# Kernel tuning notes

Hardware: AMD Instinct MI355X
Metric: run time of the kernel (lower is better)

Reference implementation:

```python
import jax, jax.numpy as jnp
import numpy as np

K_NN = 3  # pointnet2 relation default k=3


def setup_inputs() -> dict:
    key = jax.random.key(0)
    k1, k2, k3 = jax.random.split(key, 3)
    B, N, S, C = 4, 16384, 4096, 256
    q = jax.random.normal(k1, (B, N, 3), dtype=jnp.float32)
    k = jax.random.normal(k2, (B, S, 3), dtype=jnp.float32)
    v = jax.random.normal(k3, (B, S, C), dtype=jnp.float32)
    return {"q": q, "k": k, "v": v}


def reference(q, k, v):
    # squared pairwise distance: ||q||^2 - 2 q.k + ||k||^2  -> [B, N, S]
    d = (
        jnp.sum(q * q, axis=-1, keepdims=True)
        - 2.0 * jnp.einsum("bnd,bsd->bns", q, k)
        + jnp.sum(k * k, axis=-1)[:, None, :]
    )
    # 3 nearest neighbors (smallest distances)
    neg_d, idx = jax.lax.top_k(-d, K_NN)          # [B, N, 3]
    dists = -neg_d
    recip = 1.0 / (dists + 1e-8)
    weight = recip / jnp.sum(recip, axis=-1, keepdims=True)  # [B, N, 3]
    # score is zero except at idx; scatter+dense matmul == gather-weighted sum
    B = q.shape[0]
    vg = v[jnp.arange(B)[:, None, None], idx]     # [B, N, 3, C]
    extract = jnp.einsum("bnk,bnkc->bnc", weight, vg)  # [B, N, C]
    return jnp.transpose(extract, (0, 2, 1))      # [B, C, N] (embed is identity)
```

## Files before the change

### kernel.cpp

```cpp
#include <hip/hip_runtime.h>

#define BB 4
#define NN 16384
#define SS 4096
#define CC 256
#define TLD 132

typedef float f32x4 __attribute__((ext_vector_type(4)));

__device__ __forceinline__ bool lexlt(float da, int ia, float db, int ib) {
  return (da < db) || ((da == db) && (ia < ib));
}

#define DIST(kp) ({                                        \
  float _dot = (qx * (kp).x + qy * (kp).y) + qz * (kp).z;  \
  __builtin_fmaf(_dot, -2.0f, qq) + (kp).w;                \
})

#define INSERT(dd, ss) do {                                \
  bool _k2 = (dd) < d2, _k1 = (dd) < d1, _k0 = (dd) < d0;  \
  float _nd2 = __builtin_amdgcn_fmed3f((dd), d1, d2);      \
  float _nd1 = __builtin_amdgcn_fmed3f((dd), d0, d1);      \
  float _nd0 = fminf((dd), d0);                            \
  i2 = _k1 ? i1 : (_k2 ? (ss) : i2);                       \
  i1 = _k0 ? i0 : (_k1 ? (ss) : i1);                       \
  i0 = _k0 ? (ss) : i0;                                    \
  d2 = _nd2; d1 = _nd1; d0 = _nd0;                         \
} while (0)

__global__ __launch_bounds__(256, 8) void scan_kernel(
    const float* __restrict__ qg, const float* __restrict__ kg,
    float4* __restrict__ dpart, int4* __restrict__ ipart) {
#pragma clang fp contract(off)
  __shared__ __align__(16) float4 kpts[1024];
  float* md = (float*)kpts;
  int* mi = (int*)((char*)kpts + 1536);

  const int tid = threadIdx.x;
  const int blk = blockIdx.x;
  const int b = blk >> 9;
  const int seg = (blk >> 7) & 3;
  const int n0 = (blk & 127) << 7;
  const int wv = tid >> 6;
  const int lane = tid & 63;
  const int qg2 = wv & 1;
  const int half = wv >> 1;
  const int q = n0 + qg2 * 64 + lane;

  {
    const float* kb = kg + ((long)b * SS + (long)seg * 1024) * 3;
    const float4* src = (const float4*)kb + tid * 3;
    float4 f0 = src[0], f1 = src[1], f2 = src[2];
    float px[4] = {f0.x, f0.w, f1.z, f2.y};
    float py[4] = {f0.y, f1.x, f1.w, f2.z};
    float pz[4] = {f0.z, f1.y, f2.x, f2.w};
#pragma unroll
    for (int m = 0; m < 4; ++m) {
      float kk = (px[m] * px[m] + py[m] * py[m]) + pz[m] * pz[m];
      kpts[tid * 4 + m] = make_float4(px[m], py[m], pz[m], kk);
    }
  }

  const float* qp = qg + ((long)b * NN + q) * 3;
  float qx = qp[0], qy = qp[1], qz = qp[2];
  float qq = (qx * qx + qy * qy) + qz * qz;
  float d0 = 3.4e38f, d1 = 3.4e38f, d2 = 3.4e38f;
  int i0 = 0, i1 = 0, i2 = 0;
  __syncthreads();

  const int sb = seg * 1024;
  const int cbase = half << 9;

  for (int bdl = 0; bdl < 32; ++bdl) {
    const int base = cbase + (bdl << 4);
    const float tau = d2;
    float dv[16];
    unsigned msk = 0;
#pragma unroll
    for (int sj = 0; sj < 4; ++sj) {
      float4 ka = kpts[base + 4 * sj + 0];
      float4 kb_ = kpts[base + 4 * sj + 1];
      float4 kc = kpts[base + 4 * sj + 2];
      float4 kd = kpts[base + 4 * sj + 3];
      dv[4 * sj + 0] = DIST(ka);
      dv[4 * sj + 1] = DIST(kb_);
      dv[4 * sj + 2] = DIST(kc);
      dv[4 * sj + 3] = DIST(kd);
    }
#pragma unroll
    for (int j = 0; j < 16; ++j) msk |= (__any(dv[j] < tau) ? 1u : 0u) << j;
    if (msk) {
#pragma unroll
      for (int j = 0; j < 16; ++j) {
        if (msk & (1u << j)) INSERT(dv[j], sb + base + j);
      }
    }
  }

  __syncthreads();
  if (half == 1) {
    int basei = (qg2 * 64 + lane) * 3;
    md[basei + 0] = d0; md[basei + 1] = d1; md[basei + 2] = d2;
    mi[basei + 0] = i0; mi[basei + 1] = i1; mi[basei + 2] = i2;
  }
  __syncthreads();
  if (half == 0) {
    int basei = (qg2 * 64 + lane) * 3;
    float E0 = md[basei + 0], E1 = md[basei + 1], E2 = md[basei + 2];
    int F0 = mi[basei + 0], F1 = mi[basei + 1], F2 = mi[basei + 2];
    float A0 = d0, A1 = d1, A2 = d2;
    int B0 = i0, B1 = i1, B2 = i2;
    bool t = lexlt(E0, F0, A0, B0);
    float r0 = t ? E0 : A0; int s0 = t ? F0 : B0;
    float nA0 = t ? A0 : A1, nA1 = t ? A1 : A2;
    int nB0 = t ? B0 : B1, nB1 = t ? B1 : B2;
    float nE0 = t ? E1 : E0, nE1 = t ? E2 : E1;
    int nF0 = t ? F1 : F0, nF1 = t ? F2 : F1;
    bool u = lexlt(nE0, nF0, nA0, nB0);
    float r1 = u ? nE0 : nA0; int s1 = u ? nF0 : nB0;
    float mA0 = u ? nA0 : nA1; int mB0 = u ? nB0 : nB1;
    float mE0 = u ? nE1 : nE0; int mF0 = u ? nF1 : nF0;
    bool w = lexlt(mE0, mF0, mA0, mB0);
    float r2 = w ? mE0 : mA0; int s2 = w ? mF0 : mB0;
    long gid = (long)b * NN + q;
    dpart[gid * 4 + seg] = make_float4(r0, r1, r2, 0.0f);
    ipart[gid * 4 + seg] = make_int4(s0, s1, s2, 0);
  }
}

__global__ __launch_bounds__(256, 4) void gather_kernel(
    const float* __restrict__ vg, const float4* __restrict__ dpart,
    const int4* __restrict__ ipart, float* __restrict__ outg) {
#pragma clang fp contract(off)
  __shared__ __align__(16) float tile[64 * TLD];
  __shared__ float sw[64][3];
  __shared__ int si[64][3];

  const int tid = threadIdx.x;
  const int bid = blockIdx.x;
  const int xcd = bid & 7;
  const int b = xcd >> 1;
  const int chunk = xcd & 1;
  const int nblk = bid >> 3;
  const int n0 = nblk << 6;

  if (tid < 64) {
    long gid = (long)b * NN + n0 + tid;
    float D0 = 3.4e38f, D1 = 3.4e38f, D2 = 3.4e38f;
    int I0 = -1, I1 = -1, I2 = -1;
#pragma unroll
    for (int seg = 0; seg < 4; ++seg) {
      float4 dv = dpart[gid * 4 + seg];
      int4 iv = ipart[gid * 4 + seg];
      float ds_[3] = {dv.x, dv.y, dv.z};
      int is_[3] = {iv.x, iv.y, iv.z};
      for (int r = 0; r < 3; ++r) {
        float d = ds_[r];
        int s = is_[r];
        if (lexlt(d, s, D2, I2)) {
          if (lexlt(d, s, D1, I1)) {
            D2 = D1; I2 = I1;
            if (lexlt(d, s, D0, I0)) { D1 = D0; I1 = I0; D0 = d; I0 = s; }
            else { D1 = d; I1 = s; }
          } else { D2 = d; I2 = s; }
        }
      }
    }
    float r0 = 1.0f / (D0 + 1e-8f);
    float r1 = 1.0f / (D1 + 1e-8f);
    float r2 = 1.0f / (D2 + 1e-8f);
    float rs = (r0 + r1) + r2;
    sw[tid][0] = r0 / rs; sw[tid][1] = r1 / rs; sw[tid][2] = r2 / rs;
    si[tid][0] = I0; si[tid][1] = I1; si[tid][2] = I2;
  }
  __syncthreads();

  const int wv = tid >> 6;
  const int lane = tid & 63;
  const int qh = lane >> 5;
  const int slot = lane & 31;
  const float* vb = vg + (long)b * SS * CC + chunk * 128;

#pragma unroll 4
  for (int it = 0; it < 8; ++it) {
    int qs = wv * 16 + it * 2 + qh;
    float w0 = sw[qs][0], w1 = sw[qs][1], w2 = sw[qs][2];
    const float4* r0p = (const float4*)(vb + (long)si[qs][0] * CC);
    const float4* r1p = (const float4*)(vb + (long)si[qs][1] * CC);
    const float4* r2p = (const float4*)(vb + (long)si[qs][2] * CC);
    float4 a0 = r0p[slot], a1 = r1p[slot], a2 = r2p[slot];
    float4 acc;
    acc.x = (w0 * a0.x + w1 * a1.x) + w2 * a2.x;
    acc.y = (w0 * a0.y + w1 * a1.y) + w2 * a2.y;
    acc.z = (w0 * a0.z + w1 * a1.z) + w2 * a2.z;
    acc.w = (w0 * a0.w + w1 * a1.w) + w2 * a2.w;
    *(float4*)&tile[qs * TLD + slot * 4] = acc;
  }
  __syncthreads();

  {
    const int nf = tid & 15;
    const int cb0 = tid >> 4;
    const int q0 = nf << 2;
#pragma unroll 2
    for (int it = 0; it < 8; ++it) {
      int cl = cb0 + it * 16;
      int cch = (chunk << 7) + cl;
      f32x4 val;
      val.x = tile[(q0 + 0) * TLD + cl];
      val.y = tile[(q0 + 1) * TLD + cl];
      val.z = tile[(q0 + 2) * TLD + cl];
      val.w = tile[(q0 + 3) * TLD + cl];
      __builtin_nontemporal_store(
          val, (f32x4*)&outg[((long)(b * CC + cch)) * NN + n0 + q0]);
    }
  }
}

extern "C" void kernel_launch(void* const* d_in, const int* in_sizes, int n_in,
                              void* d_out, int out_size, void* d_ws, size_t ws_size,
                              hipStream_t stream) {
  const float* q = (const float*)d_in[0];
  const float* k = (const float*)d_in[1];
  const float* v = (const float*)d_in[2];
  float* out = (float*)d_out;
  float4* dpart = (float4*)d_ws;
  int4* ipart = (int4*)((char*)d_ws + (size_t)BB * NN * 4 * 16);
  hipLaunchKernelGGL(scan_kernel, dim3(2048), dim3(256), 0, stream, q, k, dpart, ipart);
  hipLaunchKernelGGL(gather_kernel, dim3(2048), dim3(256), 0, stream, v, dpart, ipart, out);
}
```

Measured before the change: 212.0 us.

## Process two queries per thread in scan kernel to reuse LDS key loads

Each thread in the kNN scan kernel now handles two query points instead of one, so every key point read from shared memory is used for two distance computations. The grid is halved to 1024 blocks, each covering 256 queries, and the shared merge buffers are resized. This cuts LDS load traffic and per-block key staging in half, at the cost of more registers (launch bounds relaxed to 4 blocks per CU), lower occupancy and fewer blocks to fill the GPU.

New measurement: 225.6 us. +6.4%, slower.

```diff
diff --git a/kernel.cpp b/kernel.cpp
--- a/kernel.cpp
+++ b/kernel.cpp
@@ -12,40 +12,41 @@
   return (da < db) || ((da == db) && (ia < ib));
 }
 
-#define DIST(kp) ({                                        \
-  float _dot = (qx * (kp).x + qy * (kp).y) + qz * (kp).z;  \
-  __builtin_fmaf(_dot, -2.0f, qq) + (kp).w;                \
+#define DIST3(QX, QY, QZ, QQ, kp) ({                            \
+  float _dot = ((QX) * (kp).x + (QY) * (kp).y) + (QZ) * (kp).z; \
+  __builtin_fmaf(_dot, -2.0f, (QQ)) + (kp).w;                   \
 })
 
-#define INSERT(dd, ss) do {                                \
-  bool _k2 = (dd) < d2, _k1 = (dd) < d1, _k0 = (dd) < d0;  \
-  float _nd2 = __builtin_amdgcn_fmed3f((dd), d1, d2);      \
-  float _nd1 = __builtin_amdgcn_fmed3f((dd), d0, d1);      \
-  float _nd0 = fminf((dd), d0);                            \
-  i2 = _k1 ? i1 : (_k2 ? (ss) : i2);                       \
-  i1 = _k0 ? i0 : (_k1 ? (ss) : i1);                       \
-  i0 = _k0 ? (ss) : i0;                                    \
-  d2 = _nd2; d1 = _nd1; d0 = _nd0;                         \
+#define INS(dd, ss, D0, D1, D2, I0, I1, I2) do {              \
+  bool _k2 = (dd) < D2, _k1 = (dd) < D1, _k0 = (dd) < D0;     \
+  float _nd2 = __builtin_amdgcn_fmed3f((dd), D1, D2);         \
+  float _nd1 = __builtin_amdgcn_fmed3f((dd), D0, D1);         \
+  float _nd0 = fminf((dd), D0);                               \
+  I2 = _k1 ? I1 : (_k2 ? (ss) : I2);                          \
+  I1 = _k0 ? I0 : (_k1 ? (ss) : I1);                          \
+  I0 = _k0 ? (ss) : I0;                                       \
+  D2 = _nd2; D1 = _nd1; D0 = _nd0;                            \
 } while (0)
 
-__global__ __launch_bounds__(256, 8) void scan_kernel(
+__global__ __launch_bounds__(256, 4) void scan_kernel(
     const float* __restrict__ qg, const float* __restrict__ kg,
     float4* __restrict__ dpart, int4* __restrict__ ipart) {
 #pragma clang fp contract(off)
   __shared__ __align__(16) float4 kpts[1024];
   float* md = (float*)kpts;
-  int* mi = (int*)((char*)kpts + 1536);
+  int* mi = (int*)((char*)kpts + 3072);
 
   const int tid = threadIdx.x;
   const int blk = blockIdx.x;
-  const int b = blk >> 9;
-  const int seg = (blk >> 7) & 3;
-  const int n0 = (blk & 127) << 7;
+  const int b = blk >> 8;
+  const int seg = (blk >> 6) & 3;
+  const int n0 = (blk & 63) << 8;
   const int wv = tid >> 6;
   const int lane = tid & 63;
   const int qg2 = wv & 1;
   const int half = wv >> 1;
-  const int q = n0 + qg2 * 64 + lane;
+  const int qA = n0 + (qg2 << 7) + lane;
+  const int qB = qA + 64;
 
   {
     const float* kb = kg + ((long)b * SS + (long)seg * 1024) * 3;
@@ -61,11 +62,16 @@
     }
   }
 
-  const float* qp = qg + ((long)b * NN + q) * 3;
-  float qx = qp[0], qy = qp[1], qz = qp[2];
-  float qq = (qx * qx + qy * qy) + qz * qz;
-  float d0 = 3.4e38f, d1 = 3.4e38f, d2 = 3.4e38f;
-  int i0 = 0, i1 = 0, i2 = 0;
+  const float* qpA = qg + ((long)b * NN + qA) * 3;
+  const float* qpB = qg + ((long)b * NN + qB) * 3;
+  float axq = qpA[0], ayq = qpA[1], azq = qpA[2];
+  float bxq = qpB[0], byq = qpB[1], bzq = qpB[2];
+  float aqq = (axq * axq + ayq * ayq) + azq * azq;
+  float bqq = (bxq * bxq + byq * byq) + bzq * bzq;
+  float ad0 = 3.4e38f, ad1 = 3.4e38f, ad2 = 3.4e38f;
+  float bd0 = 3.4e38f, bd1 = 3.4e38f, bd2 = 3.4e38f;
+  int ai0 = 0, ai1 = 0, ai2 = 0;
+  int bi0 = 0, bi1 = 0, bi2 = 0;
   __syncthreads();
 
   const int sb = seg * 1024;
@@ -73,58 +79,79 @@
 
   for (int bdl = 0; bdl < 32; ++bdl) {
     const int base = cbase + (bdl << 4);
-    const float tau = d2;
-    float dv[16];
-    unsigned msk = 0;
+    const float tauA = ad2;
+    const float tauB = bd2;
+    float dvA[16], dvB[16];
+    unsigned mskA = 0, mskB = 0;
 #pragma unroll
     for (int sj = 0; sj < 4; ++sj) {
       float4 ka = kpts[base + 4 * sj + 0];
       float4 kb_ = kpts[base + 4 * sj + 1];
       float4 kc = kpts[base + 4 * sj + 2];
       float4 kd = kpts[base + 4 * sj + 3];
-      dv[4 * sj + 0] = DIST(ka);
-      dv[4 * sj + 1] = DIST(kb_);
-      dv[4 * sj + 2] = DIST(kc);
-      dv[4 * sj + 3] = DIST(kd);
-    }
-#pragma unroll
-    for (int j = 0; j < 16; ++j) msk |= (__any(dv[j] < tau) ? 1u : 0u) << j;
-    if (msk) {
+      dvA[4 * sj + 0] = DIST3(axq, ayq, azq, aqq, ka);
+      dvB[4 * sj + 0] = DIST3(bxq, byq, bzq, bqq, ka);
+      dvA[4 * sj + 1] = DIST3(axq, ayq, azq, aqq, kb_);
+      dvB[4 * sj + 1] = DIST3(bxq, byq, bzq, bqq, kb_);
+      dvA[4 * sj + 2] = DIST3(axq, ayq, azq, aqq, kc);
+      dvB[4 * sj + 2] = DIST3(bxq, byq, bzq, bqq, kc);
+      dvA[4 * sj + 3] = DIST3(axq, ayq, azq, aqq, kd);
+      dvB[4 * sj + 3] = DIST3(bxq, byq, bzq, bqq, kd);
+    }
+#pragma unroll
+    for (int j = 0; j < 16; ++j) {
+      mskA |= (__any(dvA[j] < tauA) ? 1u : 0u) << j;
+      mskB |= (__any(dvB[j] < tauB) ? 1u : 0u) << j;
+    }
+    if (mskA) {
 #pragma unroll
       for (int j = 0; j < 16; ++j) {
-        if (msk & (1u << j)) INSERT(dv[j], sb + base + j);
+        if (mskA & (1u << j)) INS(dvA[j], sb + base + j, ad0, ad1, ad2, ai0, ai1, ai2);
       }
     }
+    if (mskB) {
+#pragma unroll
+      for (int j = 0; j < 16; ++j) {
+        if (mskB & (1u << j)) INS(dvB[j], sb + base + j, bd0, bd1, bd2, bi0, bi1, bi2);
+      }
+    }
   }
 
   __syncthreads();
   if (half == 1) {
-    int basei = (qg2 * 64 + lane) * 3;
-    md[basei + 0] = d0; md[basei + 1] = d1; md[basei + 2] = d2;
-    mi[basei + 0] = i0; mi[basei + 1] = i1; mi[basei + 2] = i2;
+    int baseA = ((qg2 << 7) + lane) * 3;
+    int baseB = baseA + 64 * 3;
+    md[baseA + 0] = ad0; md[baseA + 1] = ad1; md[baseA + 2] = ad2;
+    mi[baseA + 0] = ai0; mi[baseA + 1] = ai1; mi[baseA + 2] = ai2;
+    md[baseB + 0] = bd0; md[baseB + 1] = bd1; md[baseB + 2] = bd2;
+    mi[baseB + 0] = bi0; mi[baseB + 1] = bi1; mi[baseB + 2] = bi2;
   }
   __syncthreads();
   if (half == 0) {
-    int basei = (qg2 * 64 + lane) * 3;
-    float E0 = md[basei + 0], E1 = md[basei + 1], E2 = md[basei + 2];
-    int F0 = mi[basei + 0], F1 = mi[basei + 1], F2 = mi[basei + 2];
-    float A0 = d0, A1 = d1, A2 = d2;
-    int B0 = i0, B1 = i1, B2 = i2;
-    bool t = lexlt(E0, F0, A0, B0);
-    float r0 = t ? E0 : A0; int s0 = t ? F0 : B0;
-    float nA0 = t ? A0 : A1, nA1 = t ? A1 : A2;
-    int nB0 = t ? B0 : B1, nB1 = t ? B1 : B2;
-    float nE0 = t ? E1 : E0, nE1 = t ? E2 : E1;
-    int nF0 = t ? F1 : F0, nF1 = t ? F2 : F1;
-    bool u = lexlt(nE0, nF0, nA0, nB0);
-    float r1 = u ? nE0 : nA0; int s1 = u ? nF0 : nB0;
-    float mA0 = u ? nA0 : nA1; int mB0 = u ? nB0 : nB1;
-    float mE0 = u ? nE1 : nE0; int mF0 = u ? nF1 : nF0;
-    bool w = lexlt(mE0, mF0, mA0, mB0);
-    float r2 = w ? mE0 : mA0; int s2 = w ? mF0 : mB0;
-    long gid = (long)b * NN + q;
-    dpart[gid * 4 + seg] = make_float4(r0, r1, r2, 0.0f);
-    ipart[gid * 4 + seg] = make_int4(s0, s1, s2, 0);
+#pragma unroll
+    for (int p = 0; p < 2; ++p) {
+      int qi = (qg2 << 7) + (p ? lane + 64 : lane);
+      int basei = qi * 3;
+      float A0 = p ? bd0 : ad0, A1 = p ? bd1 : ad1, A2 = p ? bd2 : ad2;
+      int B0 = p ? bi0 : ai0, B1 = p ? bi1 : ai1, B2 = p ? bi2 : ai2;
+      float E0 = md[basei + 0], E1 = md[basei + 1], E2 = md[basei + 2];
+      int F0 = mi[basei + 0], F1 = mi[basei + 1], F2 = mi[basei + 2];
+      bool t = lexlt(E0, F0, A0, B0);
+      float r0 = t ? E0 : A0; int s0 = t ? F0 : B0;
+      float nA0 = t ? A0 : A1, nA1 = t ? A1 : A2;
+      int nB0 = t ? B0 : B1, nB1 = t ? B1 : B2;
+      float nE0 = t ? E1 : E0, nE1 = t ? E2 : E1;
+      int nF0 = t ? F1 : F0, nF1 = t ? F2 : F1;
+      bool u = lexlt(nE0, nF0, nA0, nB0);
+      float r1 = u ? nE0 : nA0; int s1 = u ? nF0 : nB0;
+      float mA0 = u ? nA0 : nA1; int mB0 = u ? nB0 : nB1;
+      float mE0 = u ? nE1 : nE0; int mF0 = u ? nF1 : nF0;
+      bool w = lexlt(mE0, mF0, mA0, mB0);
+      float r2 = w ? mE0 : mA0; int s2 = w ? mF0 : mB0;
+      long gid = (long)b * NN + n0 + qi;
+      dpart[gid * 4 + seg] = make_float4(r0, r1, r2, 0.0f);
+      ipart[gid * 4 + seg] = make_int4(s0, s1, s2, 0);
+    }
   }
 }
 
@@ -226,6 +253,6 @@
   float* out = (float*)d_out;
   float4* dpart = (float4*)d_ws;
   int4* ipart = (int4*)((char*)d_ws + (size_t)BB * NN * 4 * 16);
-  hipLaunchKernelGGL(scan_kernel, dim3(2048), dim3(256), 0, stream, q, k, dpart, ipart);
+  hipLaunchKernelGGL(scan_kernel, dim3(1024), dim3(256), 0, stream, q, k, dpart, ipart);
   hipLaunchKernelGGL(gather_kernel, dim3(2048), dim3(256), 0, stream, v, dpart, ipart, out);
 }
```
